# Kernel optimization log

Hardware: AMD Instinct MI355X
Metric: run time of the kernel (lower is better)

Reference implementation:

```python
import jax, jax.numpy as jnp
import numpy as np

NEG = 0.01  # LeakyReLU default slope
EPS = 1e-5  # InstanceNorm eps

def conv(x, w, b=None, pad=0, groups=1):
    y = jax.lax.conv_general_dilated(x, w, (1, 1), [(pad, pad), (pad, pad)],
                                     dimension_numbers=('NCHW', 'OIHW', 'NCHW'),
                                     feature_group_count=groups)
    if b is not None:
        y = y + b[None, :, None, None]
    return y

def inorm(x):
    m = jnp.mean(x, axis=(2, 3), keepdims=True)
    v = jnp.var(x, axis=(2, 3), keepdims=True)
    return (x - m) / jnp.sqrt(v + EPS)

def lrelu(x):
    return jax.nn.leaky_relu(x, NEG)

def maxpool2(x):
    return jax.lax.reduce_window(x, -jnp.inf, jax.lax.max, (1, 1, 2, 2), (1, 1, 2, 2), 'VALID')

def setup_inputs() -> dict:
    key = jax.random.key(0)
    ks = jax.random.split(key, 17)
    C = 64
    def w(k, shape, fan_in):
        return (jax.random.normal(k, shape, jnp.float32) * (1.0 / np.sqrt(fan_in)))
    return {
        'x': jax.random.normal(ks[0], (4, 3, 256, 256), jnp.float32),
        'w_proj': w(ks[1], (C, 3, 3, 3), 27), 'b_proj': jnp.zeros((C,), jnp.float32),
        'w_a1': w(ks[2], (C // 4, C, 1, 1), C), 'w_a2': w(ks[3], (C, C // 4, 1, 1), C // 4),
        'w_ref': w(ks[4], (C, 1, 3, 3), 9), 'b_ref': jnp.zeros((C,), jnp.float32),
        'w_fuse': w(ks[5], (C, C, 1, 1), C), 'b_fuse': jnp.zeros((C,), jnp.float32),
        'w_con': w(ks[6], (2 * C * 4, 1, 3, 3), 9),
        'w_u1': w(ks[7], (C, 2 * C * 4, 1, 1), 2 * C * 4), 'b_u1': jnp.zeros((C,), jnp.float32),
        'w_u2': w(ks[8], (C, C, 3, 3), 9 * C), 'b_u2': jnp.zeros((C,), jnp.float32),
        'w_sc': w(ks[9], (C, 2 * C, 1, 1), 2 * C), 'b_sc': jnp.zeros((C,), jnp.float32),
    }

def reference(x, w_proj, b_proj, w_a1, w_a2, w_ref, b_ref, w_fuse, b_fuse,
              w_con, w_u1, b_u1, w_u2, b_u2, w_sc, b_sc):
    xp = conv(x, w_proj, b_proj, pad=1)
    B, C, H, W = xp.shape
    # --- high branch: pywt wavedec2+waverec2 is perfect reconstruction (identity);
    #     torch code detaches -> stop_gradient on the reconstruction path
    xw = jax.lax.stop_gradient(xp)
    a = jnp.mean(xw, axis=(2, 3), keepdims=True)          # AdaptiveAvgPool2d(1)
    a = lrelu(conv(a, w_a1))
    a = jax.nn.sigmoid(conv(a, w_a2))
    xw = xw * a
    xw = conv(xw, w_ref, b_ref, pad=1, groups=C)          # depthwise refine
    xw = lrelu(inorm(xw))
    # --- low branch: FFT low-pass box filter
    f = jnp.fft.fftshift(jnp.fft.fft2(xp), axes=(-2, -1))
    hl = int(H * 0.3 // 2); wl = int(W * 0.3 // 2)
    hc, wc = H // 2, W // 2
    mask = jnp.zeros((H, W), bool).at[hc - hl:hc + hl, wc - wl:wc + wl].set(True)
    low = jnp.fft.ifft2(jnp.fft.ifftshift(f * mask, axes=(-2, -1))).real
    low = lrelu(inorm(conv(low, w_fuse, b_fuse)))
    # --- hypergraph construct / unwrap
    xc = jnp.concatenate([xw, low], axis=1)               # [B, 2C, H, W]
    h = conv(xc, w_con, pad=1, groups=2 * C)              # [B, 2C*k, H, W]
    u = lrelu(inorm(conv(h, w_u1, b_u1)))
    u = lrelu(inorm(conv(u, w_u2, b_u2, pad=1)))
    feat = u + conv(xc, w_sc, b_sc)
    pooled = maxpool2(feat)
    return feat, pooled
```

## Files before the change

### kernel.cpp

```cpp
#include <hip/hip_runtime.h>
#include <hip/hip_bf16.h>

#define WIDTH 256
#define HW 65536
#define IMG 16777216
#define NIMG 256
#define NSPLIT 16

typedef __attribute__((ext_vector_type(8))) short bf8v;
typedef __attribute__((ext_vector_type(4))) float f4v;

__device__ __forceinline__ float lrelu_f(float v){ return v > 0.f ? v : 0.01f*v; }
__device__ __forceinline__ unsigned short bf16u(float v){
    __hip_bfloat16 h = __float2bfloat16(v);
    return *(unsigned short*)&h;
}

__global__ __launch_bounds__(256) void k_statsf(const float* __restrict__ ps, float* __restrict__ st)
{
    const int img = threadIdx.x;
    const float* p = ps + blockIdx.x * (256 * NSPLIT * 2) + img * (NSPLIT * 2);
    float* o = st + blockIdx.x * 512;
    float S = 0.f, S2 = 0.f;
#pragma unroll
    for (int q = 0; q < NSPLIT; q++) { S += p[q * 2]; S2 += p[q * 2 + 1]; }
    const float m = S / 65536.f;
    const float var = S2 / 65536.f - m * m;
    o[img * 2]     = m;
    o[img * 2 + 1] = rsqrtf(var + 1e-5f);
}

__global__ __launch_bounds__(256) void k_attention(const float* __restrict__ ps0,
    const float* __restrict__ wa1, const float* __restrict__ wa2, float* __restrict__ a2o)
{
    __shared__ float means[256];
    __shared__ float a1s[64];
    const int tid = threadIdx.x;
    {
        const float* p = ps0 + tid * (NSPLIT * 2);
        float S = 0.f;
#pragma unroll
        for (int q = 0; q < NSPLIT; q++) S += p[q * 2];
        means[tid] = S * (1.f / 65536.f);
    }
    __syncthreads();
    if (tid < 64) {
        const int b = tid >> 4, o = tid & 15;
        float s = 0.f;
        for (int c = 0; c < 64; c++) s += wa1[o * 64 + c] * means[b * 64 + c];
        a1s[b * 16 + o] = lrelu_f(s);
    }
    __syncthreads();
    {
        const int b = tid >> 6, c = tid & 63;
        float s = 0.f;
#pragma unroll
        for (int o = 0; o < 16; o++) s += wa2[c * 16 + o] * a1s[b * 16 + o];
        a2o[tid] = 1.f / (1.f + expf(-s));
    }
}

__global__ __launch_bounds__(256, 3) void k_proj(const float* __restrict__ x,
    const float* __restrict__ wt, const float* __restrict__ bias,
    float* __restrict__ out, float* __restrict__ ps0)
{
    __shared__ float wl[3][9][32];
    const int tid = threadIdx.x;
    const int og = tid >> 5, xg = tid & 31;
    const int half = blockIdx.x & 1;
    const int y = (blockIdx.x >> 1) & 255;
    const int b = blockIdx.x >> 9;
    const int o_base = half * 32;
    const int o0l = og * 4;
    const int x0 = xg * 8;
    const int split = y & (NSPLIT - 1);

    for (int idx = tid; idx < 3 * 9 * 32; idx += 256) {
        const int o = idx & 31;
        const int rest = idx >> 5;
        const int pos = rest % 9, cc = rest / 9;
        wl[cc][pos][o] = wt[((o_base + o) * 3 + cc) * 9 + pos];
    }
    __syncthreads();

    float acc[4][8];
#pragma unroll
    for (int i = 0; i < 4; i++)
#pragma unroll
        for (int j = 0; j < 8; j++) acc[i][j] = 0.f;

#pragma unroll 2
    for (int cc = 0; cc < 3; cc++) {
        const float* src = x + ((size_t)b * 3 + cc) * HW;
#pragma unroll
        for (int dy = 0; dy < 3; dy++) {
            const int yy = y + dy - 1;
            float vv[10];
            if (yy >= 0 && yy < 256) {
                const float* r = src + (size_t)yy * WIDTH;
                vv[0] = (x0 > 0) ? r[x0 - 1] : 0.f;
                const float4 m0 = *(const float4*)(r + x0);
                const float4 m1 = *(const float4*)(r + x0 + 4);
                vv[1] = m0.x; vv[2] = m0.y; vv[3] = m0.z; vv[4] = m0.w;
                vv[5] = m1.x; vv[6] = m1.y; vv[7] = m1.z; vv[8] = m1.w;
                vv[9] = (x0 < 248) ? r[x0 + 8] : 0.f;
            } else {
#pragma unroll
                for (int q = 0; q < 10; q++) vv[q] = 0.f;
            }
#pragma unroll
            for (int dx = 0; dx < 3; dx++) {
                const float4 w4 = *(const float4*)&wl[cc][dy * 3 + dx][o0l];
                const float wv[4] = { w4.x, w4.y, w4.z, w4.w };
#pragma unroll
                for (int oi = 0; oi < 4; oi++)
#pragma unroll
                    for (int px = 0; px < 8; px++)
                        acc[oi][px] += wv[oi] * vv[px + dx];
            }
        }
    }
#pragma unroll
    for (int oi = 0; oi < 4; oi++) {
        const int o = o_base + o0l + oi;
        const float bv = bias[o];
        const size_t off = ((size_t)(b * 64 + o)) * HW + (size_t)y * WIDTH + x0;
        float4 r0, r1;
        r0.x = acc[oi][0] + bv; r0.y = acc[oi][1] + bv; r0.z = acc[oi][2] + bv; r0.w = acc[oi][3] + bv;
        r1.x = acc[oi][4] + bv; r1.y = acc[oi][5] + bv; r1.z = acc[oi][6] + bv; r1.w = acc[oi][7] + bv;
        *(float4*)(out + off) = r0;
        *(float4*)(out + off + 4) = r1;
        float s  = r0.x + r0.y + r0.z + r0.w + r1.x + r1.y + r1.z + r1.w;
        float s2 = r0.x*r0.x + r0.y*r0.y + r0.z*r0.z + r0.w*r0.w
                 + r1.x*r1.x + r1.y*r1.y + r1.z*r1.z + r1.w*r1.w;
#pragma unroll
        for (int offt = 16; offt > 0; offt >>= 1) {
            s  += __shfl_down(s, offt, 32);
            s2 += __shfl_down(s2, offt, 32);
        }
        if (xg == 0) {
            float* pp = &ps0[((b * 64 + o) * NSPLIT + split) * 2];
            atomicAdd(pp, s);
            atomicAdd(pp + 1, s2);
        }
    }
}

__global__ __launch_bounds__(256) void k_dw(const float* __restrict__ xp, const float* __restrict__ a2,
    const float* __restrict__ wref, const float* __restrict__ bref, float* __restrict__ out,
    float* __restrict__ ps1)
{
    const int tid = threadIdx.x;
    const int img = blockIdx.x >> 6;
    const int y = ((blockIdx.x & 63) << 2) + (tid >> 6);
    const int x0 = (tid & 63) * 4;
    const int c = img & 63;
    const int split = blockIdx.x & (NSPLIT - 1);
    const float* src = xp + (size_t)img * HW;
    float wv[9];
#pragma unroll
    for (int k = 0; k < 9; k++) wv[k] = wref[c * 9 + k];
    const float scale = a2[img], bb = bref[c];

    float a[4] = {0.f, 0.f, 0.f, 0.f};
#pragma unroll
    for (int dy = 0; dy < 3; dy++) {
        const int yy = y + dy - 1;
        if (yy < 0 || yy > 255) continue;
        const float* r = src + (size_t)yy * WIDTH;
        float vv[6];
        vv[0] = (x0 > 0) ? r[x0 - 1] : 0.f;
        const float4 m = *(const float4*)(r + x0);
        vv[1] = m.x; vv[2] = m.y; vv[3] = m.z; vv[4] = m.w;
        vv[5] = (x0 < 252) ? r[x0 + 4] : 0.f;
#pragma unroll
        for (int dx = 0; dx < 3; dx++)
#pragma unroll
            for (int px = 0; px < 4; px++)
                a[px] += wv[dy * 3 + dx] * vv[px + dx];
    }
    float4 o;
    o.x = bb + scale * a[0]; o.y = bb + scale * a[1];
    o.z = bb + scale * a[2]; o.w = bb + scale * a[3];
    *(float4*)(out + (size_t)img * HW + (size_t)y * WIDTH + x0) = o;

    float s  = o.x + o.y + o.z + o.w;
    float s2 = o.x*o.x + o.y*o.y + o.z*o.z + o.w*o.w;
#pragma unroll
    for (int offt = 32; offt > 0; offt >>= 1) {
        s  += __shfl_down(s, offt, 64);
        s2 += __shfl_down(s2, offt, 64);
    }
    __shared__ float ls[4][2];
    const int wid = tid >> 6, lane = tid & 63;
    if (lane == 0) { ls[wid][0] = s; ls[wid][1] = s2; }
    __syncthreads();
    if (tid == 0) {
        const float S  = ls[0][0] + ls[1][0] + ls[2][0] + ls[3][0];
        const float S2 = ls[0][1] + ls[1][1] + ls[2][1] + ls[3][1];
        float* pp = &ps1[(img * NSPLIT + split) * 2];
        atomicAdd(pp, S);
        atomicAdd(pp + 1, S2);
    }
}

__global__ void k_tables(float* __restrict__ kr2, float* __restrict__ ki2)
{
    const int t = blockIdx.x * 256 + threadIdx.x;
    if (t < 512) {
        const int tm = t & 255;
        const double PI = 3.14159265358979323846;
        const double th = 2.0 * PI * (double)tm / 256.0;
        double sr = 1.0;
        for (int k = 1; k <= 37; k++) sr += 2.0 * cos((double)k * th);
        sr += cos(38.0 * th);
        kr2[t] = (float)(sr / 256.0);
        ki2[t] = (float)(-sin(38.0 * th) / 256.0);
    }
}

__global__ __launch_bounds__(256) void k_kmat(const float* __restrict__ kr2, const float* __restrict__ ki2,
    unsigned short* __restrict__ KBr, unsigned short* __restrict__ KBi)
{
    const int n = blockIdx.x, k = threadIdx.x;
    const int d = (n - k) & 255;
    KBr[n * 256 + k] = bf16u(kr2[d]);
    KBi[n * 256 + k] = bf16u(ki2[d]);
}

__global__ __launch_bounds__(256, 2) void k_mdft1(const float* __restrict__ xp,
    const unsigned short* __restrict__ KBr, const unsigned short* __restrict__ KBi,
    unsigned short* __restrict__ TR, unsigned short* __restrict__ TI)
{
    const int tid = threadIdx.x, lane = tid & 63, wave = tid >> 6;
    const int img = blockIdx.x >> 2;
    const int mb = (blockIdx.x >> 1) & 1, nb = blockIdx.x & 1;
    const int M0 = mb * 128 + (wave >> 1) * 64;
    const int N0 = nb * 128 + (wave & 1) * 64;
    const int lrow = lane & 15, lk = lane >> 4;
    const float* Xb = xp + (size_t)img * HW;

    f4v aR[4][4], aI[4][4];
#pragma unroll
    for (int m = 0; m < 4; m++)
#pragma unroll
        for (int n = 0; n < 4; n++) { aR[m][n] = (f4v){0,0,0,0}; aI[m][n] = (f4v){0,0,0,0}; }

#pragma unroll 1
    for (int k0 = 0; k0 < 256; k0 += 32) {
        bf8v af[4];
#pragma unroll
        for (int m = 0; m < 4; m++) {
            const float* rp = Xb + (size_t)(M0 + m * 16 + lrow) * 256 + k0 + lk * 8;
            const float4 a0 = *(const float4*)rp;
            const float4 a1 = *(const float4*)(rp + 4);
            bf8v t;
            t[0] = (short)bf16u(a0.x); t[1] = (short)bf16u(a0.y);
            t[2] = (short)bf16u(a0.z); t[3] = (short)bf16u(a0.w);
            t[4] = (short)bf16u(a1.x); t[5] = (short)bf16u(a1.y);
            t[6] = (short)bf16u(a1.z); t[7] = (short)bf16u(a1.w);
            af[m] = t;
        }
#pragma unroll
        for (int n = 0; n < 4; n++) {
            const int xcol = N0 + n * 16 + lrow;
            const bf8v br = *(const bf8v*)(KBr + xcol * 256 + k0 + lk * 8);
            const bf8v bi = *(const bf8v*)(KBi + xcol * 256 + k0 + lk * 8);
#pragma unroll
            for (int m = 0; m < 4; m++) {
                aR[m][n] = __builtin_amdgcn_mfma_f32_16x16x32_bf16(af[m], br, aR[m][n], 0, 0, 0);
                aI[m][n] = __builtin_amdgcn_mfma_f32_16x16x32_bf16(af[m], bi, aI[m][n], 0, 0, 0);
            }
        }
    }
#pragma unroll
    for (int n = 0; n < 4; n++) {
        const size_t xoff = (size_t)img * HW + (size_t)(N0 + n * 16 + lrow) * 256;
#pragma unroll
        for (int m = 0; m < 4; m++) {
            const size_t off = xoff + M0 + m * 16 + lk * 4;
            const f4v r = aR[m][n], ii = aI[m][n];
            ushort4 ur, ui;
            ur.x = bf16u(r[0]); ur.y = bf16u(r[1]); ur.z = bf16u(r[2]); ur.w = bf16u(r[3]);
            ui.x = bf16u(ii[0]); ui.y = bf16u(ii[1]); ui.z = bf16u(ii[2]); ui.w = bf16u(ii[3]);
            *(ushort4*)(TR + off) = ur;
            *(ushort4*)(TI + off) = ui;
        }
    }
}

__global__ __launch_bounds__(256, 2) void k_mdft2(const unsigned short* __restrict__ TR,
    const unsigned short* __restrict__ TI, const unsigned short* __restrict__ KBr,
    const unsigned short* __restrict__ KBi, float* __restrict__ low)
{
    const int tid = threadIdx.x, lane = tid & 63, wave = tid >> 6;
    const int img = blockIdx.x >> 2;
    const int mb = (blockIdx.x >> 1) & 1, nb = blockIdx.x & 1;
    const int M0 = mb * 128 + (wave >> 1) * 64;
    const int N0 = nb * 128 + (wave & 1) * 64;
    const int lrow = lane & 15, lk = lane >> 4;
    const unsigned short* TRb = TR + (size_t)img * HW;
    const unsigned short* TIb = TI + (size_t)img * HW;

    f4v aR[4][4], aI[4][4];
#pragma unroll
    for (int m = 0; m < 4; m++)
#pragma unroll
        for (int n = 0; n < 4; n++) { aR[m][n] = (f4v){0,0,0,0}; aI[m][n] = (f4v){0,0,0,0}; }

#pragma unroll 1
    for (int k0 = 0; k0 < 256; k0 += 32) {
        bf8v afR[4], afI[4];
#pragma unroll
        for (int m = 0; m < 4; m++) {
            const int ro = (M0 + m * 16 + lrow) * 256 + k0 + lk * 8;
            afR[m] = *(const bf8v*)(TRb + ro);
            afI[m] = *(const bf8v*)(TIb + ro);
        }
#pragma unroll
        for (int n = 0; n < 4; n++) {
            const int ycol = N0 + n * 16 + lrow;
            const bf8v br = *(const bf8v*)(KBr + ycol * 256 + k0 + lk * 8);
            const bf8v bi = *(const bf8v*)(KBi + ycol * 256 + k0 + lk * 8);
#pragma unroll
            for (int m = 0; m < 4; m++) {
                aR[m][n] = __builtin_amdgcn_mfma_f32_16x16x32_bf16(afR[m], br, aR[m][n], 0, 0, 0);
                aI[m][n] = __builtin_amdgcn_mfma_f32_16x16x32_bf16(afI[m], bi, aI[m][n], 0, 0, 0);
            }
        }
    }
#pragma unroll
    for (int n = 0; n < 4; n++) {
        const size_t yoff = (size_t)img * HW + (size_t)(N0 + n * 16 + lrow) * 256;
#pragma unroll
        for (int m = 0; m < 4; m++) {
            const f4v r = aR[m][n], ii = aI[m][n];
            const float4 v = make_float4(r[0] - ii[0], r[1] - ii[1], r[2] - ii[2], r[3] - ii[3]);
            *(float4*)(low + yoff + M0 + m * 16 + lk * 4) = v;
        }
    }
}

__global__ __launch_bounds__(256) void k_weff_bf(const float* __restrict__ w_u1,
    const float* __restrict__ w_con, unsigned short* __restrict__ wbf)
{
    const int f = blockIdx.x * 256 + threadIdx.x;
    if (f >= 73728) return;
    const int ch = f & 31, oc = (f >> 5) & 63, cp = f >> 11;
    const int pos = cp % 9, cb = cp / 9;
    const int g = cb * 32 + ch;
    float s = 0.f;
#pragma unroll
    for (int j = 0; j < 4; j++) s += w_u1[oc * 512 + g * 4 + j] * w_con[(g * 4 + j) * 9 + pos];
    wbf[f] = bf16u(s);
}

template<int CIN>
__global__ __launch_bounds__(256) void k_wcvt(const float* __restrict__ w, unsigned short* __restrict__ wbf)
{
    const int f = blockIdx.x * 256 + threadIdx.x;
    if (f >= 64 * CIN * 9) return;
    const int ch = f & 31, oc = (f >> 5) & 63, cp = f >> 11;
    const int pos = cp % 9, cb = cp / 9;
    const int c = cb * 32 + ch;
    wbf[f] = bf16u(w[oc * CIN * 9 + c * 9 + pos]);
}

template<int CIN>
__global__ __launch_bounds__(256, 2) void k_mconv(
    const float* __restrict__ in0, const float* __restrict__ in1,
    const unsigned short* __restrict__ wbf, const float* __restrict__ bias,
    float* __restrict__ out,
    const float* __restrict__ stA, const float* __restrict__ stB,
    float* __restrict__ psOut)
{
    __shared__ unsigned short Xl[4 * 260 * 32];
    __shared__ float sh_ms[64];
    __shared__ float red[4][64][2];
    const int tid = threadIdx.x;
    const int lane = tid & 63;
    const int wave = tid >> 6;
    const int b = blockIdx.x >> 7;
    const int y0 = (blockIdx.x & 127) * 2;
    const int row_sel = wave >> 1;
    const int px_base = (wave & 1) * 128;
    const int split = blockIdx.x & (NSPLIT - 1);

    for (int i = tid; i < 4 * 260 * 32 / 2; i += 256) ((unsigned int*)Xl)[i] = 0u;

    f4v acc[8][4];
#pragma unroll
    for (int i = 0; i < 8; i++)
#pragma unroll
        for (int n = 0; n < 4; n++) acc[i][n] = (f4v){0.f, 0.f, 0.f, 0.f};

    const int pxl   = px_base + (lane & 15);
    const int gsl   = lane >> 4;
    const int wlane = (lane & 15) * 32 + gsl * 8;

    constexpr int NC = CIN / 32;
#pragma unroll 1
    for (int cb = 0; cb < NC; cb++) {
        const int c0 = cb * 32;
        const bool second = (CIN == 128 && c0 >= 64);
        const float* src = (second ? in1 : in0) + ((size_t)b * 64 + (c0 & 63)) * HW;
        const float* st = second ? stB : stA;
        __syncthreads();
        if (tid < 32) {
            const int img = b * 64 + (c0 & 63) + tid;
            sh_ms[tid * 2]     = st[img * 2];
            sh_ms[tid * 2 + 1] = st[img * 2 + 1];
        }
        __syncthreads();
        {
            const int px = tid;
            const int px_idx = px + 1;
            const int sw = (px_idx >> 1) & 3;
#pragma unroll 1
            for (int r = 0; r < 4; r++) {
                const int yy = y0 - 1 + r;
                if (yy < 0 || yy > 255) continue;
                const float* rp = src + (size_t)yy * WIDTH + px;
#pragma unroll 4
                for (int d = 0; d < 16; d++) {
                    float va = rp[(size_t)(2 * d) * HW];
                    float vb = rp[(size_t)(2 * d + 1) * HW];
                    va = lrelu_f((va - sh_ms[4 * d])     * sh_ms[4 * d + 1]);
                    vb = lrelu_f((vb - sh_ms[4 * d + 2]) * sh_ms[4 * d + 3]);
                    const unsigned int dw = (unsigned int)bf16u(va)
                                          | ((unsigned int)bf16u(vb) << 16);
                    const int byte = r * 16640 + px_idx * 64
                                   + (((d >> 2) ^ sw) << 4) + ((d & 3) << 2);
                    *(unsigned int*)((char*)Xl + byte) = dw;
                }
            }
        }
        __syncthreads();
#pragma unroll 1
        for (int pos = 0; pos < 9; pos++) {
            const int dy = pos / 3, dx = pos - dy * 3;
            const unsigned short* wp = wbf + (cb * 9 + pos) * 2048 + wlane;
            const bf8v wf0 = *(const bf8v*)(wp);
            const bf8v wf1 = *(const bf8v*)(wp + 512);
            const bf8v wf2 = *(const bf8v*)(wp + 1024);
            const bf8v wf3 = *(const bf8v*)(wp + 1536);
            const int pxe = pxl + dx;
            const int row = row_sel + dy;
            const char* abase = (const char*)Xl + row * 16640 + pxe * 64
                              + ((gsl ^ ((pxe >> 1) & 3)) << 4);
#pragma unroll
            for (int i = 0; i < 8; i++) {
                const bf8v af = *(const bf8v*)(abase + i * 1024);
                acc[i][0] = __builtin_amdgcn_mfma_f32_16x16x32_bf16(af, wf0, acc[i][0], 0, 0, 0);
                acc[i][1] = __builtin_amdgcn_mfma_f32_16x16x32_bf16(af, wf1, acc[i][1], 0, 0, 0);
                acc[i][2] = __builtin_amdgcn_mfma_f32_16x16x32_bf16(af, wf2, acc[i][2], 0, 0, 0);
                acc[i][3] = __builtin_amdgcn_mfma_f32_16x16x32_bf16(af, wf3, acc[i][3], 0, 0, 0);
            }
        }
    }
    const int yrow = y0 + row_sel;
    const int lrow = lane & 15, lk = lane >> 4;
#pragma unroll
    for (int n = 0; n < 4; n++) {
        const float bv = bias[n * 16 + lrow];
        float* po = out + ((size_t)(b * 64) + n * 16 + lrow) * HW
                  + (size_t)yrow * WIDTH + px_base + lk * 4;
        float s = 0.f, s2 = 0.f;
#pragma unroll
        for (int i = 0; i < 8; i++) {
            const f4v a = acc[i][n];
            float4 v;
            v.x = a[0] + bv; v.y = a[1] + bv; v.z = a[2] + bv; v.w = a[3] + bv;
            s  += v.x + v.y + v.z + v.w;
            s2 += v.x*v.x + v.y*v.y + v.z*v.z + v.w*v.w;
            *(float4*)(po + i * 16) = v;
        }
        s  += __shfl_down(s, 32);  s  += __shfl_down(s, 16);
        s2 += __shfl_down(s2, 32); s2 += __shfl_down(s2, 16);
        if (lk == 0) { red[wave][n * 16 + lrow][0] = s; red[wave][n * 16 + lrow][1] = s2; }
    }
    __syncthreads();
    if (tid < 64) {
        const float S  = red[0][tid][0] + red[1][tid][0] + red[2][tid][0] + red[3][tid][0];
        const float S2 = red[0][tid][1] + red[1][tid][1] + red[2][tid][1] + red[3][tid][1];
        float* pp = &psOut[((b * 64 + tid) * NSPLIT + split) * 2];
        atomicAdd(pp, S);
        atomicAdd(pp + 1, S2);
    }
}

template<int CIN, bool ADD, bool NORMIN, bool STATS>
__global__ __launch_bounds__(256, 4) void k_conv1(
    const float* __restrict__ in0, const float* __restrict__ in1,
    const float* __restrict__ wt, const float* __restrict__ bias,
    const float* __restrict__ addsrc, float* __restrict__ out,
    const float* __restrict__ stA, const float* __restrict__ stB,
    const float* __restrict__ stAdd, float* __restrict__ psOut)
{
    __shared__ float wl[CIN][64];
    const int tid = threadIdx.x;
    const int og = tid >> 5;
    const int pg = tid & 31;
    const int y = blockIdx.x & 255;
    const int b = blockIdx.x >> 8;
    const int x0 = pg * 8;
    const int o0 = og * 8;
    const int split = blockIdx.x & (NSPLIT - 1);

    for (int idx = tid; idx < CIN * 64; idx += 256) {
        const int o = idx & 63, c = idx >> 6;
        wl[c][o] = wt[o * CIN + c];
    }
    __syncthreads();

    float acc[8][8];
#pragma unroll
    for (int i = 0; i < 8; i++)
#pragma unroll
        for (int j = 0; j < 8; j++) acc[i][j] = 0.f;

    {
        const float* p = in0 + ((size_t)b * 64) * HW + (size_t)y * WIDTH + x0;
#pragma unroll 2
        for (int c = 0; c < 64; c++) {
            const float4 v0 = *(const float4*)(p + (size_t)c * HW);
            const float4 v1 = *(const float4*)(p + (size_t)c * HW + 4);
            float vv[8] = { v0.x, v0.y, v0.z, v0.w, v1.x, v1.y, v1.z, v1.w };
            if constexpr (NORMIN) {
                const float mm = stA[(b * 64 + c) * 2], ss = stA[(b * 64 + c) * 2 + 1];
#pragma unroll
                for (int j = 0; j < 8; j++) vv[j] = lrelu_f((vv[j] - mm) * ss);
            }
            const float4 wA = *(const float4*)&wl[c][o0];
            const float4 wB = *(const float4*)&wl[c][o0 + 4];
            const float wv[8] = { wA.x, wA.y, wA.z, wA.w, wB.x, wB.y, wB.z, wB.w };
#pragma unroll
            for (int oi = 0; oi < 8; oi++)
#pragma unroll
                for (int px = 0; px < 8; px++)
                    acc[oi][px] += wv[oi] * vv[px];
        }
    }
    if constexpr (CIN == 128) {
        const float* p = in1 + ((size_t)b * 64) * HW + (size_t)y * WIDTH + x0;
#pragma unroll 2
        for (int c = 0; c < 64; c++) {
            const float4 v0 = *(const float4*)(p + (size_t)c * HW);
            const float4 v1 = *(const float4*)(p + (size_t)c * HW + 4);
            float vv[8] = { v0.x, v0.y, v0.z, v0.w, v1.x, v1.y, v1.z, v1.w };
            if constexpr (NORMIN) {
                const float mm = stB[(b * 64 + c) * 2], ss = stB[(b * 64 + c) * 2 + 1];
#pragma unroll
                for (int j = 0; j < 8; j++) vv[j] = lrelu_f((vv[j] - mm) * ss);
            }
            const float4 wA = *(const float4*)&wl[64 + c][o0];
            const float4 wB = *(const float4*)&wl[64 + c][o0 + 4];
            const float wv[8] = { wA.x, wA.y, wA.z, wA.w, wB.x, wB.y, wB.z, wB.w };
#pragma unroll
            for (int oi = 0; oi < 8; oi++)
#pragma unroll
                for (int px = 0; px < 8; px++)
                    acc[oi][px] += wv[oi] * vv[px];
        }
    }

#pragma unroll
    for (int oi = 0; oi < 8; oi++) {
        const int o = o0 + oi;
        const float bv = bias[o];
        const size_t off = ((size_t)(b * 64 + o)) * HW + (size_t)y * WIDTH + x0;
        float r[8];
#pragma unroll
        for (int j = 0; j < 8; j++) r[j] = acc[oi][j] + bv;
        if constexpr (ADD) {
            const float4 a0 = *(const float4*)(addsrc + off);
            const float4 a1 = *(const float4*)(addsrc + off + 4);
            float av[8] = { a0.x, a0.y, a0.z, a0.w, a1.x, a1.y, a1.z, a1.w };
            const float mm = stAdd[(b * 64 + o) * 2], ss = stAdd[(b * 64 + o) * 2 + 1];
#pragma unroll
            for (int j = 0; j < 8; j++) r[j] += lrelu_f((av[j] - mm) * ss);
        }
        float4 r0 = make_float4(r[0], r[1], r[2], r[3]);
        float4 r1 = make_float4(r[4], r[5], r[6], r[7]);
        *(float4*)(out + off) = r0;
        *(float4*)(out + off + 4) = r1;
        if constexpr (STATS) {
            float s = 0.f, s2 = 0.f;
#pragma unroll
            for (int j = 0; j < 8; j++) { s += r[j]; s2 += r[j] * r[j]; }
#pragma unroll
            for (int offt = 16; offt > 0; offt >>= 1) {
                s  += __shfl_down(s, offt, 32);
                s2 += __shfl_down(s2, offt, 32);
            }
            if (pg == 0) {
                float* pp = &psOut[((b * 64 + o) * NSPLIT + split) * 2];
                atomicAdd(pp, s);
                atomicAdd(pp + 1, s2);
            }
        }
    }
}

__global__ __launch_bounds__(256) void k_maxpool(const float* __restrict__ feat, float* __restrict__ out)
{
    const int idx = blockIdx.x * 256 + threadIdx.x;
    const int xo = idx & 127;
    const int yo = (idx >> 7) & 127;
    const int img = idx >> 14;
    const float* p = feat + (size_t)img * HW + (size_t)(yo * 2) * WIDTH + xo * 2;
    out[idx] = fmaxf(fmaxf(p[0], p[1]), fmaxf(p[WIDTH], p[WIDTH + 1]));
}

extern "C" void kernel_launch(void* const* d_in, const int* in_sizes, int n_in,
                              void* d_out, int out_size, void* d_ws, size_t ws_size,
                              hipStream_t stream)
{
    const float* x      = (const float*)d_in[0];
    const float* w_proj = (const float*)d_in[1];
    const float* b_proj = (const float*)d_in[2];
    const float* w_a1   = (const float*)d_in[3];
    const float* w_a2   = (const float*)d_in[4];
    const float* w_ref  = (const float*)d_in[5];
    const float* b_ref  = (const float*)d_in[6];
    const float* w_fuse = (const float*)d_in[7];
    const float* b_fuse = (const float*)d_in[8];
    const float* w_con  = (const float*)d_in[9];
    const float* w_u1   = (const float*)d_in[10];
    const float* b_u1   = (const float*)d_in[11];
    const float* w_u2   = (const float*)d_in[12];
    const float* b_u2   = (const float*)d_in[13];
    const float* w_sc   = (const float*)d_in[14];
    const float* b_sc   = (const float*)d_in[15];

    float* wsf  = (float*)d_ws;
    float* buf0 = wsf;
    float* buf1 = wsf + (size_t)IMG;
    float* buf2 = wsf + (size_t)2 * IMG;
    float* aux  = wsf + (size_t)3 * IMG;
    float* a2b  = aux;
    float* kr2  = aux + 256;
    float* ki2  = aux + 768;
    unsigned short* wbfA = (unsigned short*)(aux + 1280);
    unsigned short* wbfB = wbfA + 73728;
    unsigned short* KBr  = wbfB + 36864;
    unsigned short* KBi  = KBr + 65536;
    float* ps   = aux + 1280 + 120832;
    float* st   = ps + 5 * 256 * NSPLIT * 2;

    float* fout = (float*)d_out;
    float* pout = fout + (size_t)IMG;
    unsigned short* T1R = (unsigned short*)buf2;
    unsigned short* T1I = T1R + (size_t)IMG;

    const int PSSLOT = 256 * NSPLIT * 2;

    hipMemsetAsync(ps, 0, 5 * PSSLOT * sizeof(float), stream);
    k_tables<<<2, 256, 0, stream>>>(kr2, ki2);
    k_kmat<<<256, 256, 0, stream>>>(kr2, ki2, KBr, KBi);
    k_weff_bf<<<288, 256, 0, stream>>>(w_u1, w_con, wbfA);
    k_wcvt<64><<<144, 256, 0, stream>>>(w_u2, wbfB);
    k_proj<<<2048, 256, 0, stream>>>(x, w_proj, b_proj, buf0, ps);
    k_attention<<<1, 256, 0, stream>>>(ps, w_a1, w_a2, a2b);
    k_dw<<<16384, 256, 0, stream>>>(buf0, a2b, w_ref, b_ref, buf1, ps + PSSLOT);
    k_mdft1<<<1024, 256, 0, stream>>>(buf0, KBr, KBi, T1R, T1I);
    k_mdft2<<<1024, 256, 0, stream>>>(T1R, T1I, KBr, KBi, fout);
    k_conv1<64, false, false, true><<<1024, 256, 0, stream>>>(
        fout, nullptr, w_fuse, b_fuse, nullptr, buf0,
        nullptr, nullptr, nullptr, ps + 2 * PSSLOT);
    k_statsf<<<2, 256, 0, stream>>>(ps + PSSLOT, st + 512);
    k_mconv<128><<<512, 256, 0, stream>>>(buf1, buf0, wbfA, b_u1, fout,
        st + 512, st + 1024, ps + 3 * PSSLOT);
    k_statsf<<<1, 256, 0, stream>>>(ps + 3 * PSSLOT, st + 1536);
    k_mconv<64><<<512, 256, 0, stream>>>(fout, nullptr, wbfB, b_u2, buf2,
        st + 1536, st + 1536, ps + 4 * PSSLOT);
    k_statsf<<<1, 256, 0, stream>>>(ps + 4 * PSSLOT, st + 2048);
    k_conv1<128, true, true, false><<<1024, 256, 0, stream>>>(
        buf1, buf0, w_sc, b_sc, buf2, fout,
        st + 512, st + 1024, st + 2048, nullptr);
    k_maxpool<<<16384, 256, 0, stream>>>(fout, pout);
}
```

Before: 567.8 us.

## Port 1x1 convolutions to bf16 MFMA with swizzled LDS staging

Replaces the scalar FP32 1x1 conv kernel with an MFMA-based kernel that stages each row's input channels as bf16 in swizzled shared memory and reads pre-converted bf16 weights. It adds small weight conversion kernels and uses block-level reduction for instance-norm statistics. The aim is to move the 1x1 conv arithmetic onto matrix cores. In exchange it lowers input and weight precision to bf16 and drops occupancy hints from 4 to 2 blocks.

```diff
diff --git a/kernel.cpp b/kernel.cpp
--- a/kernel.cpp
+++ b/kernel.cpp
@@ -364,6 +364,15 @@
     const int pos = cp % 9, cb = cp / 9;
     const int c = cb * 32 + ch;
     wbf[f] = bf16u(w[oc * CIN * 9 + c * 9 + pos]);
+}
+
+template<int CIN>
+__global__ __launch_bounds__(256) void k_wcvt1(const float* __restrict__ w, unsigned short* __restrict__ wbf)
+{
+    const int f = blockIdx.x * 256 + threadIdx.x;
+    if (f >= 64 * CIN) return;
+    const int ch = f & 31, oc = (f >> 5) & 63, cb = f >> 11;
+    wbf[f] = bf16u(w[oc * CIN + cb * 32 + ch]);
 }
 
 template<int CIN>
@@ -490,114 +499,122 @@
 }
 
 template<int CIN, bool ADD, bool NORMIN, bool STATS>
-__global__ __launch_bounds__(256, 4) void k_conv1(
+__global__ __launch_bounds__(256, 2) void k_pconv(
     const float* __restrict__ in0, const float* __restrict__ in1,
-    const float* __restrict__ wt, const float* __restrict__ bias,
+    const unsigned short* __restrict__ wbf, const float* __restrict__ bias,
     const float* __restrict__ addsrc, float* __restrict__ out,
     const float* __restrict__ stA, const float* __restrict__ stB,
     const float* __restrict__ stAdd, float* __restrict__ psOut)
 {
-    __shared__ float wl[CIN][64];
-    const int tid = threadIdx.x;
-    const int og = tid >> 5;
-    const int pg = tid & 31;
-    const int y = blockIdx.x & 255;
-    const int b = blockIdx.x >> 8;
-    const int x0 = pg * 8;
-    const int o0 = og * 8;
+    __shared__ unsigned short Xl[256 * 32];
+    __shared__ float sh_ms[64];
+    __shared__ float red[4][64][2];
+    const int tid = threadIdx.x, lane = tid & 63, wave = tid >> 6;
+    const int y = blockIdx.x & 255, b = blockIdx.x >> 8;
     const int split = blockIdx.x & (NSPLIT - 1);
-
-    for (int idx = tid; idx < CIN * 64; idx += 256) {
-        const int o = idx & 63, c = idx >> 6;
-        wl[c][o] = wt[o * CIN + c];
-    }
-    __syncthreads();
-
-    float acc[8][8];
-#pragma unroll
-    for (int i = 0; i < 8; i++)
-#pragma unroll
-        for (int j = 0; j < 8; j++) acc[i][j] = 0.f;
-
-    {
-        const float* p = in0 + ((size_t)b * 64) * HW + (size_t)y * WIDTH + x0;
-#pragma unroll 2
-        for (int c = 0; c < 64; c++) {
-            const float4 v0 = *(const float4*)(p + (size_t)c * HW);
-            const float4 v1 = *(const float4*)(p + (size_t)c * HW + 4);
-            float vv[8] = { v0.x, v0.y, v0.z, v0.w, v1.x, v1.y, v1.z, v1.w };
-            if constexpr (NORMIN) {
-                const float mm = stA[(b * 64 + c) * 2], ss = stA[(b * 64 + c) * 2 + 1];
-#pragma unroll
-                for (int j = 0; j < 8; j++) vv[j] = lrelu_f((vv[j] - mm) * ss);
-            }
-            const float4 wA = *(const float4*)&wl[c][o0];
-            const float4 wB = *(const float4*)&wl[c][o0 + 4];
-            const float wv[8] = { wA.x, wA.y, wA.z, wA.w, wB.x, wB.y, wB.z, wB.w };
-#pragma unroll
-            for (int oi = 0; oi < 8; oi++)
-#pragma unroll
-                for (int px = 0; px < 8; px++)
-                    acc[oi][px] += wv[oi] * vv[px];
-        }
-    }
-    if constexpr (CIN == 128) {
-        const float* p = in1 + ((size_t)b * 64) * HW + (size_t)y * WIDTH + x0;
-#pragma unroll 2
-        for (int c = 0; c < 64; c++) {
-            const float4 v0 = *(const float4*)(p + (size_t)c * HW);
-            const float4 v1 = *(const float4*)(p + (size_t)c * HW + 4);
-            float vv[8] = { v0.x, v0.y, v0.z, v0.w, v1.x, v1.y, v1.z, v1.w };
-            if constexpr (NORMIN) {
-                const float mm = stB[(b * 64 + c) * 2], ss = stB[(b * 64 + c) * 2 + 1];
-#pragma unroll
-                for (int j = 0; j < 8; j++) vv[j] = lrelu_f((vv[j] - mm) * ss);
-            }
-            const float4 wA = *(const float4*)&wl[64 + c][o0];
-            const float4 wB = *(const float4*)&wl[64 + c][o0 + 4];
-            const float wv[8] = { wA.x, wA.y, wA.z, wA.w, wB.x, wB.y, wB.z, wB.w };
-#pragma unroll
-            for (int oi = 0; oi < 8; oi++)
-#pragma unroll
-                for (int px = 0; px < 8; px++)
-                    acc[oi][px] += wv[oi] * vv[px];
-        }
-    }
-
-#pragma unroll
-    for (int oi = 0; oi < 8; oi++) {
-        const int o = o0 + oi;
-        const float bv = bias[o];
-        const size_t off = ((size_t)(b * 64 + o)) * HW + (size_t)y * WIDTH + x0;
-        float r[8];
-#pragma unroll
-        for (int j = 0; j < 8; j++) r[j] = acc[oi][j] + bv;
-        if constexpr (ADD) {
-            const float4 a0 = *(const float4*)(addsrc + off);
-            const float4 a1 = *(const float4*)(addsrc + off + 4);
-            float av[8] = { a0.x, a0.y, a0.z, a0.w, a1.x, a1.y, a1.z, a1.w };
-            const float mm = stAdd[(b * 64 + o) * 2], ss = stAdd[(b * 64 + o) * 2 + 1];
-#pragma unroll
-            for (int j = 0; j < 8; j++) r[j] += lrelu_f((av[j] - mm) * ss);
-        }
-        float4 r0 = make_float4(r[0], r[1], r[2], r[3]);
-        float4 r1 = make_float4(r[4], r[5], r[6], r[7]);
-        *(float4*)(out + off) = r0;
-        *(float4*)(out + off + 4) = r1;
+    const int lrow = lane & 15, gsl = lane >> 4;
+    const int wpx = wave * 64;
+    const int wlane = lrow * 32 + gsl * 8;
+
+    f4v acc[4][4];
+#pragma unroll
+    for (int m = 0; m < 4; m++)
+#pragma unroll
+        for (int n = 0; n < 4; n++) acc[m][n] = (f4v){0.f, 0.f, 0.f, 0.f};
+
+    constexpr int NC = CIN / 32;
+#pragma unroll 1
+    for (int cb = 0; cb < NC; cb++) {
+        const int c0 = cb * 32;
+        const bool second = (CIN == 128 && c0 >= 64);
+        const float* src = (second ? in1 : in0) + ((size_t)b * 64 + (c0 & 63)) * HW
+                         + (size_t)y * WIDTH;
+        __syncthreads();
+        if (NORMIN && tid < 32) {
+            const float* st = second ? stB : stA;
+            const int img = b * 64 + (c0 & 63) + tid;
+            sh_ms[tid * 2]     = st[img * 2];
+            sh_ms[tid * 2 + 1] = st[img * 2 + 1];
+        }
+        __syncthreads();
+        {
+            const int px = tid;
+            const int sw = (px >> 1) & 3;
+#pragma unroll 4
+            for (int d = 0; d < 16; d++) {
+                float va = src[(size_t)(2 * d) * HW + px];
+                float vb = src[(size_t)(2 * d + 1) * HW + px];
+                if constexpr (NORMIN) {
+                    va = lrelu_f((va - sh_ms[4 * d])     * sh_ms[4 * d + 1]);
+                    vb = lrelu_f((vb - sh_ms[4 * d + 2]) * sh_ms[4 * d + 3]);
+                }
+                const unsigned int dw = (unsigned int)bf16u(va)
+                                      | ((unsigned int)bf16u(vb) << 16);
+                const int byte = px * 64 + (((d >> 2) ^ sw) << 4) + ((d & 3) << 2);
+                *(unsigned int*)((char*)Xl + byte) = dw;
+            }
+        }
+        __syncthreads();
+        {
+            const unsigned short* wp = wbf + cb * 2048 + wlane;
+            const bf8v wf0 = *(const bf8v*)(wp);
+            const bf8v wf1 = *(const bf8v*)(wp + 512);
+            const bf8v wf2 = *(const bf8v*)(wp + 1024);
+            const bf8v wf3 = *(const bf8v*)(wp + 1536);
+#pragma unroll
+            for (int m = 0; m < 4; m++) {
+                const int px = wpx + m * 16 + lrow;
+                const char* abase = (const char*)Xl + px * 64
+                                  + ((gsl ^ ((px >> 1) & 3)) << 4);
+                const bf8v af = *(const bf8v*)abase;
+                acc[m][0] = __builtin_amdgcn_mfma_f32_16x16x32_bf16(af, wf0, acc[m][0], 0, 0, 0);
+                acc[m][1] = __builtin_amdgcn_mfma_f32_16x16x32_bf16(af, wf1, acc[m][1], 0, 0, 0);
+                acc[m][2] = __builtin_amdgcn_mfma_f32_16x16x32_bf16(af, wf2, acc[m][2], 0, 0, 0);
+                acc[m][3] = __builtin_amdgcn_mfma_f32_16x16x32_bf16(af, wf3, acc[m][3], 0, 0, 0);
+            }
+        }
+    }
+    const int lk = gsl;
+#pragma unroll
+    for (int n = 0; n < 4; n++) {
+        const int oc = n * 16 + lrow;
+        const float bv = bias[oc];
+        float mm = 0.f, ss = 0.f;
+        if constexpr (ADD) { mm = stAdd[(b * 64 + oc) * 2]; ss = stAdd[(b * 64 + oc) * 2 + 1]; }
+        const size_t orow = ((size_t)(b * 64 + oc)) * HW + (size_t)y * WIDTH;
+        float s = 0.f, s2 = 0.f;
+#pragma unroll
+        for (int m = 0; m < 4; m++) {
+            const int px = wpx + m * 16 + lk * 4;
+            const f4v a = acc[m][n];
+            float r[4] = { a[0] + bv, a[1] + bv, a[2] + bv, a[3] + bv };
+            if constexpr (ADD) {
+                const float4 av = *(const float4*)(addsrc + orow + px);
+                r[0] += lrelu_f((av.x - mm) * ss);
+                r[1] += lrelu_f((av.y - mm) * ss);
+                r[2] += lrelu_f((av.z - mm) * ss);
+                r[3] += lrelu_f((av.w - mm) * ss);
+            }
+            *(float4*)(out + orow + px) = make_float4(r[0], r[1], r[2], r[3]);
+            if constexpr (STATS) {
+                s  += r[0] + r[1] + r[2] + r[3];
+                s2 += r[0]*r[0] + r[1]*r[1] + r[2]*r[2] + r[3]*r[3];
+            }
+        }
         if constexpr (STATS) {
-            float s = 0.f, s2 = 0.f;
-#pragma unroll
-            for (int j = 0; j < 8; j++) { s += r[j]; s2 += r[j] * r[j]; }
-#pragma unroll
-            for (int offt = 16; offt > 0; offt >>= 1) {
-                s  += __shfl_down(s, offt, 32);
-                s2 += __shfl_down(s2, offt, 32);
-            }
-            if (pg == 0) {
-                float* pp = &psOut[((b * 64 + o) * NSPLIT + split) * 2];
-                atomicAdd(pp, s);
-                atomicAdd(pp + 1, s2);
-            }
+            s  += __shfl_down(s, 32);  s  += __shfl_down(s, 16);
+            s2 += __shfl_down(s2, 32); s2 += __shfl_down(s2, 16);
+            if (lk == 0) { red[wave][oc][0] = s; red[wave][oc][1] = s2; }
+        }
+    }
+    if constexpr (STATS) {
+        __syncthreads();
+        if (tid < 64) {
+            const float S  = red[0][tid][0] + red[1][tid][0] + red[2][tid][0] + red[3][tid][0];
+            const float S2 = red[0][tid][1] + red[1][tid][1] + red[2][tid][1] + red[3][tid][1];
+            float* pp = &psOut[((b * 64 + tid) * NSPLIT + split) * 2];
+            atomicAdd(pp, S);
+            atomicAdd(pp + 1, S2);
         }
     }
 }
@@ -645,7 +662,9 @@
     unsigned short* wbfB = wbfA + 73728;
     unsigned short* KBr  = wbfB + 36864;
     unsigned short* KBi  = KBr + 65536;
-    float* ps   = aux + 1280 + 120832;
+    unsigned short* wbfF = KBi + 65536;
+    unsigned short* wbfS = wbfF + 4096;
+    float* ps   = aux + 1280 + 120832 + 6144;
     float* st   = ps + 5 * 256 * NSPLIT * 2;
 
     float* fout = (float*)d_out;
@@ -660,13 +679,15 @@
     k_kmat<<<256, 256, 0, stream>>>(kr2, ki2, KBr, KBi);
     k_weff_bf<<<288, 256, 0, stream>>>(w_u1, w_con, wbfA);
     k_wcvt<64><<<144, 256, 0, stream>>>(w_u2, wbfB);
+    k_wcvt1<64><<<16, 256, 0, stream>>>(w_fuse, wbfF);
+    k_wcvt1<128><<<32, 256, 0, stream>>>(w_sc, wbfS);
     k_proj<<<2048, 256, 0, stream>>>(x, w_proj, b_proj, buf0, ps);
     k_attention<<<1, 256, 0, stream>>>(ps, w_a1, w_a2, a2b);
     k_dw<<<16384, 256, 0, stream>>>(buf0, a2b, w_ref, b_ref, buf1, ps + PSSLOT);
     k_mdft1<<<1024, 256, 0, stream>>>(buf0, KBr, KBi, T1R, T1I);
     k_mdft2<<<1024, 256, 0, stream>>>(T1R, T1I, KBr, KBi, fout);
-    k_conv1<64, false, false, true><<<1024, 256, 0, stream>>>(
-        fout, nullptr, w_fuse, b_fuse, nullptr, buf0,
+    k_pconv<64, false, false, true><<<1024, 256, 0, stream>>>(
+        fout, nullptr, wbfF, b_fuse, nullptr, buf0,
         nullptr, nullptr, nullptr, ps + 2 * PSSLOT);
     k_statsf<<<2, 256, 0, stream>>>(ps + PSSLOT, st + 512);
     k_mconv<128><<<512, 256, 0, stream>>>(buf1, buf0, wbfA, b_u1, fout,
@@ -675,8 +696,8 @@
     k_mconv<64><<<512, 256, 0, stream>>>(fout, nullptr, wbfB, b_u2, buf2,
         st + 1536, st + 1536, ps + 4 * PSSLOT);
     k_statsf<<<1, 256, 0, stream>>>(ps + 4 * PSSLOT, st + 2048);
-    k_conv1<128, true, true, false><<<1024, 256, 0, stream>>>(
-        buf1, buf0, w_sc, b_sc, buf2, fout,
+    k_pconv<128, true, true, false><<<1024, 256, 0, stream>>>(
+        buf1, buf0, wbfS, b_sc, buf2, fout,
         st + 512, st + 1024, st + 2048, nullptr);
     k_maxpool<<<16384, 256, 0, stream>>>(fout, pout);
 }
```

New measurement: 493.3 us. -13.1%, faster.
